# Kernel tuning notes

Measured on AMD Instinct MI355X. Metric: run time of the kernel, lower is better.

Reference implementation:

```python
import jax, jax.numpy as jnp
import numpy as np

N_QUBITS = 8
N_LAYERS = 4
BATCH = 4096


def _ry(theta):
    # RY(theta) = [[cos(t/2), -sin(t/2)], [sin(t/2), cos(t/2)]]
    c = jnp.cos(theta / 2).astype(jnp.complex64)
    s = jnp.sin(theta / 2).astype(jnp.complex64)
    return jnp.stack([jnp.stack([c, -s], axis=-1),
                      jnp.stack([s, c], axis=-1)], axis=-2)  # (..., 2, 2)


def _rz(theta):
    # RZ(theta) = diag(exp(-i t/2), exp(+i t/2))
    p = jnp.exp(-0.5j * theta.astype(jnp.complex64))
    z = jnp.zeros_like(p)
    return jnp.stack([jnp.stack([p, z], axis=-1),
                      jnp.stack([z, jnp.conj(p)], axis=-1)], axis=-2)


def _apply_1q(state, U, w):
    # state: (B, 2, 2, ..., 2); apply 2x2 unitary U on wire w (axis 1+w).
    st = jnp.moveaxis(state, 1 + w, -1)
    if U.ndim == 3:  # per-sample (batched) gate, U: (B, 2, 2)
        st = jnp.einsum('bij,b...j->b...i', U, st)
    else:            # shared gate, U: (2, 2)
        st = jnp.einsum('ij,b...j->b...i', U, st)
    return jnp.moveaxis(st, -1, 1 + w)


def _apply_cnot(state, c, t):
    # flip target wire t where control wire c is |1>
    st = jnp.moveaxis(state, (1 + c, 1 + t), (-2, -1))
    st = jnp.concatenate([st[..., 0:1, :], st[..., 1:2, ::-1]], axis=-2)
    return jnp.moveaxis(st, (-2, -1), (1 + c, 1 + t))


def _circuit(x, weights):
    B = x.shape[0]
    state = jnp.zeros((B,) + (2,) * N_QUBITS, jnp.complex64)
    state = state.at[(slice(None),) + (0,) * N_QUBITS].set(1.0)  # |0...0>
    # Angle encoding: RY(x_i) on each wire, batched over samples
    for i in range(N_QUBITS):
        state = _apply_1q(state, _ry(x[:, i]), i)
    # Variational layers: CNOT ring then RY/RZ rotations
    for l in range(N_LAYERS):
        for i in range(N_QUBITS):
            state = _apply_cnot(state, i, (i + 1) % N_QUBITS)
        for i in range(N_QUBITS):
            state = _apply_1q(state, _ry(weights[l, i, 0]), i)
            state = _apply_1q(state, _rz(weights[l, i, 1]), i)
    # <Z_0> = P(q0=0) - P(q0=1)
    probs = jnp.sum(jnp.abs(state.reshape(B, 2, -1)) ** 2, axis=-1)
    return (probs[:, 0] - probs[:, 1]).astype(jnp.float32)


def setup_inputs() -> dict:
    key = jax.random.key(0)
    k1, k2 = jax.random.split(key)
    x = jax.random.uniform(k1, (BATCH, N_QUBITS), dtype=jnp.float32) * jnp.pi
    weights = jax.random.normal(k2, (N_LAYERS, N_QUBITS, 2), dtype=jnp.float32) * 0.1
    return {"x": x, "weights": weights}


def reference(x, weights):
    return _circuit(x, weights)
```

## Files before the change

### kernel.cpp

```cpp
#include <hip/hip_runtime.h>

#define NQ 8
#define NL 4
#define BATCH 4096


template <int CTRL>
__device__ __forceinline__ float dppx(float v) {
  return __int_as_float(
      __builtin_amdgcn_update_dpp(0, __float_as_int(v), CTRL, 0xF, 0xF, true));
}

__device__ __forceinline__ float swz16(float v) {
  return __int_as_float(__builtin_amdgcn_ds_swizzle(__float_as_int(v), 0x401F));
}
__device__ __forceinline__ float swz4(float v) {
  return __int_as_float(__builtin_amdgcn_ds_swizzle(__float_as_int(v), 0x101F));
}
__device__ __forceinline__ float bperm(int addr, float v) {
  return __int_as_float(__builtin_amdgcn_ds_bpermute(addr, __float_as_int(v)));
}

template <int W>
__device__ __forceinline__ float xl(float v, int bp32) {
  if constexpr (W == 0) return bperm(bp32, v);
  else if constexpr (W == 1) return swz16(v);
  else if constexpr (W == 2) return dppx<0x128>(v);
  else if constexpr (W == 3) return swz4(v);
  else if constexpr (W == 4) return dppx<0x4E>(v);
  else return dppx<0xB1>(v);
}

template <int W>
__device__ __forceinline__ void ry_gate(float re[4], float im[4],
                                        float c, float s, int lane, int bp32) {
  if constexpr (W <= 5) {
    const float ss = ((lane >> (5 - W)) & 1) ? s : -s;
#pragma unroll
    for (int r = 0; r < 4; ++r) {
      float pr = xl<W>(re[r], bp32);
      float pi = xl<W>(im[r], bp32);
      re[r] = c * re[r] + ss * pr;
      im[r] = c * im[r] + ss * pi;
    }
  } else {
    constexpr int m = 1 << (7 - W);
#pragma unroll
    for (int r = 0; r < 4; ++r) {
      if ((r & m) == 0) {
        const int r1 = r | m;
        float a0r = re[r], a1r = re[r1];
        float a0i = im[r], a1i = im[r1];
        re[r]  = c * a0r - s * a1r;
        re[r1] = s * a0r + c * a1r;
        im[r]  = c * a0i - s * a1i;
        im[r1] = s * a0i + c * a1i;
      }
    }
  }
}

template <int W>
__device__ __forceinline__ void rz_gate(float re[4], float im[4],
                                        float c, float s, int lane) {
  if constexpr (W <= 5) {
    const float ss = ((lane >> (5 - W)) & 1) ? s : -s;
#pragma unroll
    for (int r = 0; r < 4; ++r) {
      float nr = re[r] * c - im[r] * ss;
      float ni = im[r] * c + re[r] * ss;
      re[r] = nr; im[r] = ni;
    }
  } else {
    constexpr int m = 1 << (7 - W);
#pragma unroll
    for (int r = 0; r < 4; ++r) {
      const float ss = (r & m) ? s : -s;
      float nr = re[r] * c - im[r] * ss;
      float ni = im[r] * c + re[r] * ss;
      re[r] = nr; im[r] = ni;
    }
  }
}

__device__ __forceinline__ void ring(float re[4], float im[4],
                                     int addr_e, int addr_o, bool p2) {
  const float t0r = p2 ? re[2] : re[0];
  const float t1r = p2 ? re[3] : re[1];
  const float t2r = p2 ? re[1] : re[3];
  const float t3r = p2 ? re[0] : re[2];
  const float t0i = p2 ? im[2] : im[0];
  const float t1i = p2 ? im[3] : im[1];
  const float t2i = p2 ? im[1] : im[3];
  const float t3i = p2 ? im[0] : im[2];
  re[0] = bperm(addr_e, t0r);
  re[1] = bperm(addr_o, t1r);
  re[2] = bperm(addr_e, t2r);
  re[3] = bperm(addr_o, t3r);
  im[0] = bperm(addr_e, t0i);
  im[1] = bperm(addr_o, t1i);
  im[2] = bperm(addr_e, t2i);
  im[3] = bperm(addr_o, t3i);
}

__global__ __launch_bounds__(256, 4) void vqc_kernel(const float* __restrict__ x,
                                                     const float* __restrict__ w,
                                                     float* __restrict__ out) {
  const int lane = (int)(threadIdx.x & 63);
  const int s = (int)((blockIdx.x * blockDim.x + threadIdx.x) >> 6);

  const int gray   = lane ^ (lane >> 1);
  const int addr_e = gray << 2;
  const int addr_o = addr_e ^ 0xC0;
  const bool p2    = (__popc(lane) & 1) != 0;
  const int bp32   = (lane ^ 32) << 2;

  float re[4] = {0.f, 0.f, 0.f, 0.f};
  float im[4] = {0.f, 0.f, 0.f, 0.f};
  if (lane == 0) re[0] = 1.f;

  {
    const float4 x0 = *(const float4*)&x[s * 8];
    const float4 x1 = *(const float4*)&x[s * 8 + 4];
    float c, sn;
    __sincosf(x0.x * 0.5f, &sn, &c); ry_gate<0>(re, im, c, sn, lane, bp32);
    __sincosf(x0.y * 0.5f, &sn, &c); ry_gate<1>(re, im, c, sn, lane, bp32);
    __sincosf(x0.z * 0.5f, &sn, &c); ry_gate<2>(re, im, c, sn, lane, bp32);
    __sincosf(x0.w * 0.5f, &sn, &c); ry_gate<3>(re, im, c, sn, lane, bp32);
    __sincosf(x1.x * 0.5f, &sn, &c); ry_gate<4>(re, im, c, sn, lane, bp32);
    __sincosf(x1.y * 0.5f, &sn, &c); ry_gate<5>(re, im, c, sn, lane, bp32);
    __sincosf(x1.z * 0.5f, &sn, &c); ry_gate<6>(re, im, c, sn, lane, bp32);
    __sincosf(x1.w * 0.5f, &sn, &c); ry_gate<7>(re, im, c, sn, lane, bp32);
  }

#pragma unroll
  for (int l = 0; l < NL - 1; ++l) {
    ring(re, im, addr_e, addr_o, p2);
    const float* wl = &w[l * NQ * 2];
#define APPLY_ROT(W) { float cy, sy, cz, sz;            \
    __sincosf(wl[(W) * 2 + 0] * 0.5f, &sy, &cy);        \
    __sincosf(wl[(W) * 2 + 1] * 0.5f, &sz, &cz);        \
    ry_gate<W>(re, im, cy, sy, lane, bp32);             \
    rz_gate<W>(re, im, cz, sz, lane); }
    APPLY_ROT(0) APPLY_ROT(1) APPLY_ROT(2) APPLY_ROT(3)
    APPLY_ROT(4) APPLY_ROT(5) APPLY_ROT(6) APPLY_ROT(7)
#undef APPLY_ROT
  }

  ring(re, im, addr_e, addr_o, p2);
  {
    float cy, sy;
    __sincosf(w[(NL - 1) * NQ * 2 + 0] * 0.5f, &sy, &cy);
    ry_gate<0>(re, im, cy, sy, lane, bp32);
  }

  float acc = 0.f;
#pragma unroll
  for (int r = 0; r < 4; ++r) acc += re[r] * re[r] + im[r] * im[r];
  acc = (lane & 32) ? -acc : acc;
  acc += dppx<0xB1>(acc);
  acc += dppx<0x4E>(acc);
  acc += swz4(acc);
  acc += dppx<0x128>(acc);
  acc += swz16(acc);
  acc += bperm(bp32, acc);
  if (lane == 0) out[s] = acc;
}

extern "C" void kernel_launch(void* const* d_in, const int* in_sizes, int n_in,
                              void* d_out, int out_size, void* d_ws, size_t ws_size,
                              hipStream_t stream) {
  const float* x = (const float*)d_in[0];
  const float* w = (const float*)d_in[1];
  float* out = (float*)d_out;
  (void)in_sizes; (void)n_in; (void)out_size; (void)d_ws; (void)ws_size;

  dim3 grid(BATCH * 64 / 256), block(256);
  hipLaunchKernelGGL(vqc_kernel, grid, block, 0, stream, x, w, out);
}
```

Baseline: 63.90 us.

## Build encoded product state analytically and fuse first CNOT ring into layout

The eight batched RY encoding gates are replaced by a closed-form product-state amplitude. Each lane computes its amplitudes as products of cos/sin of the input angles, indexed through the Gray-code permutation so that the first CNOT ring is absorbed into the initial layout. The first layer's wire-0 RY/RZ is also specialised for a purely real state. This removes many cross-lane shuffles and FMAs from the encoding stage, at the cost of more intricate index logic that must exactly match the ring permutation.

```diff
diff --git a/kernel.cpp b/kernel.cpp
--- a/kernel.cpp
+++ b/kernel.cpp
@@ -115,37 +115,77 @@
   const bool p2    = (__popc(lane) & 1) != 0;
   const int bp32   = (lane ^ 32) << 2;
 
-  float re[4] = {0.f, 0.f, 0.f, 0.f};
-  float im[4] = {0.f, 0.f, 0.f, 0.f};
-  if (lane == 0) re[0] = 1.f;
-
+  float fc[8], fs[8];
   {
     const float4 x0 = *(const float4*)&x[s * 8];
     const float4 x1 = *(const float4*)&x[s * 8 + 4];
-    float c, sn;
-    __sincosf(x0.x * 0.5f, &sn, &c); ry_gate<0>(re, im, c, sn, lane, bp32);
-    __sincosf(x0.y * 0.5f, &sn, &c); ry_gate<1>(re, im, c, sn, lane, bp32);
-    __sincosf(x0.z * 0.5f, &sn, &c); ry_gate<2>(re, im, c, sn, lane, bp32);
-    __sincosf(x0.w * 0.5f, &sn, &c); ry_gate<3>(re, im, c, sn, lane, bp32);
-    __sincosf(x1.x * 0.5f, &sn, &c); ry_gate<4>(re, im, c, sn, lane, bp32);
-    __sincosf(x1.y * 0.5f, &sn, &c); ry_gate<5>(re, im, c, sn, lane, bp32);
-    __sincosf(x1.z * 0.5f, &sn, &c); ry_gate<6>(re, im, c, sn, lane, bp32);
-    __sincosf(x1.w * 0.5f, &sn, &c); ry_gate<7>(re, im, c, sn, lane, bp32);
-  }
-
-#pragma unroll
-  for (int l = 0; l < NL - 1; ++l) {
+    __sincosf(x0.x * 0.5f, &fs[0], &fc[0]);
+    __sincosf(x0.y * 0.5f, &fs[1], &fc[1]);
+    __sincosf(x0.z * 0.5f, &fs[2], &fc[2]);
+    __sincosf(x0.w * 0.5f, &fs[3], &fc[3]);
+    __sincosf(x1.x * 0.5f, &fs[4], &fc[4]);
+    __sincosf(x1.y * 0.5f, &fs[5], &fc[5]);
+    __sincosf(x1.z * 0.5f, &fs[6], &fc[6]);
+    __sincosf(x1.w * 0.5f, &fs[7], &fc[7]);
+  }
+
+  float re[4], im[4];
+  {
+    const int L0  = lane & 1;
+    const int L5b = (lane >> 5) & 1;
+    const float g2 = (gray & 1) ? fs[5] : fc[5];
+    const float g3 = (gray & 2) ? fs[4] : fc[4];
+    const float g4 = (gray & 4) ? fs[3] : fc[3];
+    const float g5 = (gray & 8) ? fs[2] : fc[2];
+    const float Pl = (g2 * g3) * (g4 * g5);
+    const int  b6 = ((lane >> 4) & 1) ^ L5b;
+    const float h0 = (b6  ? fs[1] : fc[1]) * (L5b ? fs[0] : fc[0]);
+    const float h1 = (b6  ? fc[1] : fs[1]) * (L5b ? fc[0] : fs[0]);
+    const float A0 = Pl * h0, A1 = Pl * h1;
+    const float f6a = L0 ? fs[6] : fc[6];
+    const float f6b = L0 ? fc[6] : fs[6];
+    re[0] = A0 * fc[7] * f6a;
+    re[1] = A1 * fs[7] * f6a;
+    re[2] = A0 * fs[7] * f6b;
+    re[3] = A1 * fc[7] * f6b;
+    im[0] = 0.f; im[1] = 0.f; im[2] = 0.f; im[3] = 0.f;
+  }
+
+#define APPLY_ROT(WL, W) { float cy, sy, cz, sz;         \
+    __sincosf((WL)[(W) * 2 + 0] * 0.5f, &sy, &cy);       \
+    __sincosf((WL)[(W) * 2 + 1] * 0.5f, &sz, &cz);       \
+    ry_gate<W>(re, im, cy, sy, lane, bp32);              \
+    rz_gate<W>(re, im, cz, sz, lane); }
+
+  {
+    const float* wl = &w[0];
+    float cy, sy, cz, sz;
+    __sincosf(wl[0] * 0.5f, &sy, &cy);
+    __sincosf(wl[1] * 0.5f, &sz, &cz);
+    const float ssy = (lane & 32) ? sy : -sy;
+#pragma unroll
+    for (int r = 0; r < 4; ++r) {
+      float p = bperm(bp32, re[r]);
+      re[r] = cy * re[r] + ssy * p;
+    }
+    const float ssz = (lane & 32) ? sz : -sz;
+#pragma unroll
+    for (int r = 0; r < 4; ++r) {
+      im[r] = ssz * re[r];
+      re[r] = cz * re[r];
+    }
+    APPLY_ROT(wl, 1) APPLY_ROT(wl, 2) APPLY_ROT(wl, 3)
+    APPLY_ROT(wl, 4) APPLY_ROT(wl, 5) APPLY_ROT(wl, 6) APPLY_ROT(wl, 7)
+  }
+
+#pragma unroll
+  for (int l = 1; l < NL - 1; ++l) {
     ring(re, im, addr_e, addr_o, p2);
     const float* wl = &w[l * NQ * 2];
-#define APPLY_ROT(W) { float cy, sy, cz, sz;            \
-    __sincosf(wl[(W) * 2 + 0] * 0.5f, &sy, &cy);        \
-    __sincosf(wl[(W) * 2 + 1] * 0.5f, &sz, &cz);        \
-    ry_gate<W>(re, im, cy, sy, lane, bp32);             \
-    rz_gate<W>(re, im, cz, sz, lane); }
-    APPLY_ROT(0) APPLY_ROT(1) APPLY_ROT(2) APPLY_ROT(3)
-    APPLY_ROT(4) APPLY_ROT(5) APPLY_ROT(6) APPLY_ROT(7)
+    APPLY_ROT(wl, 0) APPLY_ROT(wl, 1) APPLY_ROT(wl, 2) APPLY_ROT(wl, 3)
+    APPLY_ROT(wl, 4) APPLY_ROT(wl, 5) APPLY_ROT(wl, 6) APPLY_ROT(wl, 7)
+  }
 #undef APPLY_ROT
-  }
 
   ring(re, im, addr_e, addr_o, p2);
   {
```

Result: no change. 63.01 us (-1.4%).
